# Kernel optimization log

Measured on AMD Instinct MI355X. Metric: run time of the kernel, lower is better.

Reference implementation:

```python
import jax, jax.numpy as jnp
import numpy as np

N = 50000          # nodes
E = 1600000        # edges (avg degree 32)
D_IN = 128
D_OUT = 128
NEG_SLOPE = 0.01   # F.leaky_relu default (module ignores its negative_slope attr)


def setup_inputs() -> dict:
    key = jax.random.key(0)
    k = jax.random.split(key, 7)
    h = jax.random.normal(k[0], (N, D_IN), dtype=jnp.float32)
    embedding = jax.random.normal(k[1], (N, D_OUT), dtype=jnp.float32)
    # params (xavier-ish scaling)
    W_lin = jax.random.normal(k[2], (D_OUT, D_IN), dtype=jnp.float32) * (2.0 / (D_IN + D_OUT)) ** 0.5
    w_fc = jax.random.normal(k[3], (1, 2 * D_OUT), dtype=jnp.float32) * (2.0 / (2 * D_OUT + 1)) ** 0.5
    w_emb = jax.random.normal(k[4], (1, 2 * D_OUT), dtype=jnp.float32) * (2.0 / (2 * D_OUT + 1)) ** 0.5
    src = jax.random.randint(k[5], (E,), 0, N, dtype=jnp.int64 if jax.config.jax_enable_x64 else jnp.int32)
    dst = jax.random.randint(k[6], (E,), 0, N, dtype=jnp.int64 if jax.config.jax_enable_x64 else jnp.int32)
    return {"h": h, "embedding": embedding, "W_lin": W_lin, "w_fc": w_fc,
            "w_emb": w_emb, "src": src, "dst": dst}


def reference(h, embedding, W_lin, w_fc, w_emb, src, dst):
    n = h.shape[0]
    d = W_lin.shape[0]
    # z = lin(h): [N, out]
    z = h @ W_lin.T
    # attn_fc(cat(z_src, z_dst)) + attn_embed(cat(e_src, e_dst)) split into per-node
    # scalar scores so we gather [E] scalars instead of materializing [E, 2*out].
    s_fc_src = z @ w_fc[0, :d]            # [N]
    s_fc_dst = z @ w_fc[0, d:]            # [N]
    s_em_src = embedding @ w_emb[0, :d]   # [N]
    s_em_dst = embedding @ w_emb[0, d:]   # [N]
    a = (s_fc_src + s_em_src)[src] + (s_fc_dst + s_em_dst)[dst]   # [E]
    e = jnp.where(a > 0, a, NEG_SLOPE * a)  # leaky_relu, slope 0.01
    # segment softmax over incoming edges of each dst node
    m = jax.ops.segment_max(e, dst, num_segments=n)               # [N]
    e_exp = jnp.exp(e - m[dst])                                   # [E]
    denom = jax.ops.segment_sum(e_exp, dst, num_segments=n)       # [N]
    alpha = e_exp / denom[dst]                                    # [E]
    # weighted neighbor aggregation: h_out[v] = sum_{(u->v)} alpha * z[u]
    h_out = jax.ops.segment_sum(alpha[:, None] * z[src], dst, num_segments=n)
    return h_out
```

## Files before the change

kernel.cpp:

```cpp
#include <hip/hip_runtime.h>
#include <hip/hip_bf16.h>

#define D 128
#define BSH 7
#define BDST 128
#define NCH 256
#define CAP 6144

typedef __attribute__((ext_vector_type(8))) short short8;
typedef __attribute__((ext_vector_type(4))) float f32x4;

__device__ __forceinline__ unsigned short f2bf(float f) {
  unsigned u = __float_as_uint(f);
  unsigned r = (u + 0x7FFFu + ((u >> 16) & 1u)) >> 16;
  return (unsigned short)r;
}

__global__ __launch_bounds__(256) void k_wconv(const float* __restrict__ W,
                                               unsigned short* __restrict__ Wb) {
  const int i = blockIdx.x * 256 + threadIdx.x;
  float4 f = ((const float4*)W)[i];
  ushort4 o;
  o.x = f2bf(f.x); o.y = f2bf(f.y); o.z = f2bf(f.z); o.w = f2bf(f.w);
  ((ushort4*)Wb)[i] = o;
}

__global__ __launch_bounds__(256) void k_lin(const float* __restrict__ h,
                                             const unsigned short* __restrict__ Wb,
                                             const float* __restrict__ w_fc,
                                             unsigned* __restrict__ zd,
                                             float* __restrict__ sfc_s,
                                             float* __restrict__ sfc_d, int n) {
  const int lane = threadIdx.x & 63;
  const int wid = threadIdx.x >> 6;
  const int m0 = blockIdx.x * 64 + wid * 16;
  if (m0 >= n) return;
  const int c = lane & 15;
  const int g = lane >> 4;

  int arow = m0 + c;
  if (arow >= n) arow = n - 1;
  const float4* hrow = (const float4*)(h + (size_t)arow * 128);

  short8 afr[4];
#pragma unroll
  for (int s = 0; s < 4; ++s) {
    float4 f0 = hrow[8 * s + 2 * g];
    float4 f1 = hrow[8 * s + 2 * g + 1];
    short8 a;
    a[0] = (short)f2bf(f0.x); a[1] = (short)f2bf(f0.y);
    a[2] = (short)f2bf(f0.z); a[3] = (short)f2bf(f0.w);
    a[4] = (short)f2bf(f1.x); a[5] = (short)f2bf(f1.y);
    a[6] = (short)f2bf(f1.z); a[7] = (short)f2bf(f1.w);
    afr[s] = a;
  }

  f32x4 acc[8];
#pragma unroll
  for (int t = 0; t < 8; ++t) acc[t] = (f32x4){0.f, 0.f, 0.f, 0.f};

#pragma unroll
  for (int s = 0; s < 4; ++s) {
#pragma unroll
    for (int t = 0; t < 8; ++t) {
      short8 b = *(const short8*)(Wb + ((size_t)(t * 16 + c) * 128 + 32 * s + 8 * g));
      acc[t] = __builtin_amdgcn_mfma_f32_16x16x32_bf16(afr[s], b, acc[t], 0, 0, 0);
    }
  }

  float wfs[8], wfd[8];
#pragma unroll
  for (int t = 0; t < 8; ++t) {
    wfs[t] = w_fc[t * 16 + c];
    wfd[t] = w_fc[128 + t * 16 + c];
  }

  const int rbase = m0 + 4 * g;
#pragma unroll
  for (int r = 0; r < 4; ++r) {
    const int row = rbase + r;
    if (row < n) {
#pragma unroll
      for (int tp = 0; tp < 4; ++tp) {
        unsigned dw = ((unsigned)f2bf(acc[tp + 4][r]) << 16) | (unsigned)f2bf(acc[tp][r]);
        zd[(size_t)row * 64 + tp * 16 + c] = dw;
      }
    }
    float ps = 0.f, pd = 0.f;
#pragma unroll
    for (int t = 0; t < 8; ++t) {
      ps += acc[t][r] * wfs[t];
      pd += acc[t][r] * wfd[t];
    }
#pragma unroll
    for (int off = 1; off < 16; off <<= 1) {
      ps += __shfl_xor(ps, off, 64);
      pd += __shfl_xor(pd, off, 64);
    }
    if (c == 0 && row < n) {
      sfc_s[row] = ps;
      sfc_d[row] = pd;
    }
  }
}

__global__ __launch_bounds__(256) void k_scal(const float* __restrict__ emb,
                                              const float* __restrict__ w_emb,
                                              const float* __restrict__ sfc_s,
                                              const float* __restrict__ sfc_d,
                                              float* __restrict__ a_src,
                                              float* __restrict__ a_dst, int n) {
  const int lane = threadIdx.x & 63;
  const int v = blockIdx.x * 4 + (threadIdx.x >> 6);
  if (v >= n) return;
  float2 ee = ((const float2*)emb)[(size_t)v * 64 + lane];
  float2 wes = ((const float2*)w_emb)[lane];
  float2 wed = ((const float2*)w_emb)[64 + lane];
  float ssrc = ee.x * wes.x + ee.y * wes.y;
  float sdst = ee.x * wed.x + ee.y * wed.y;
#pragma unroll
  for (int off = 32; off; off >>= 1) {
    ssrc += __shfl_xor(ssrc, off, 64);
    sdst += __shfl_xor(sdst, off, 64);
  }
  if (lane == 0) {
    a_src[v] = ssrc + sfc_s[v];
    a_dst[v] = sdst + sfc_d[v];
  }
}

__global__ __launch_bounds__(256) void k_chist(const int* __restrict__ dst,
                                               int* __restrict__ cnt,
                                               int E, int NB, int CHSZ) {
  __shared__ int hl[512];
  const int tid = threadIdx.x, c = blockIdx.x;
  for (int i = tid; i < NB; i += 256) hl[i] = 0;
  __syncthreads();
  const int beg = c * CHSZ, end = min(beg + CHSZ, E);
  for (int i = beg + tid; i < end; i += 256) atomicAdd(&hl[dst[i] >> BSH], 1);
  __syncthreads();
  for (int b = tid; b < NB; b += 256) cnt[(size_t)b * NCH + c] = hl[b];
}

__global__ __launch_bounds__(256) void ks1(const int* __restrict__ cnt,
                                           int* __restrict__ partial, int M) {
  const int tid = threadIdx.x;
  const int t0 = blockIdx.x * 1024 + tid * 4;
  int s = 0;
  if (t0 + 3 < M) {
    int4 v = *(const int4*)(cnt + t0);
    s = v.x + v.y + v.z + v.w;
  } else {
    for (int j = 0; j < 4; ++j)
      if (t0 + j < M) s += cnt[t0 + j];
  }
#pragma unroll
  for (int off = 32; off; off >>= 1) s += __shfl_xor(s, off, 64);
  __shared__ int w[4];
  if ((tid & 63) == 0) w[tid >> 6] = s;
  __syncthreads();
  if (tid == 0) partial[blockIdx.x] = w[0] + w[1] + w[2] + w[3];
}

__global__ __launch_bounds__(256) void ks2(const int* __restrict__ partial,
                                           int* __restrict__ chunk_off, int P) {
  __shared__ int s[256];
  const int tid = threadIdx.x;
  int v = (tid < P) ? partial[tid] : 0;
  s[tid] = v;
  __syncthreads();
  for (int off = 1; off < 256; off <<= 1) {
    int a = (tid >= off) ? s[tid - off] : 0;
    __syncthreads();
    s[tid] += a;
    __syncthreads();
  }
  if (tid < P) chunk_off[tid] = s[tid] - v;
}

__global__ __launch_bounds__(256) void ks3(int* __restrict__ cnt,
                                           const int* __restrict__ chunk_off, int M) {
  const int tid = threadIdx.x;
  const int t0 = blockIdx.x * 1024 + tid * 4;
  int v[4];
  int s = 0;
#pragma unroll
  for (int j = 0; j < 4; ++j) {
    v[j] = (t0 + j < M) ? cnt[t0 + j] : 0;
    s += v[j];
  }
  __shared__ int sh[256];
  sh[tid] = s;
  __syncthreads();
  for (int off = 1; off < 256; off <<= 1) {
    int a = (tid >= off) ? sh[tid - off] : 0;
    __syncthreads();
    sh[tid] += a;
    __syncthreads();
  }
  int excl = chunk_off[blockIdx.x] + sh[tid] - s;
#pragma unroll
  for (int j = 0; j < 4; ++j) {
    if (t0 + j < M) cnt[t0 + j] = excl;
    excl += v[j];
  }
}

__global__ __launch_bounds__(256) void k_cscat(const int* __restrict__ src,
                                               const int* __restrict__ dst,
                                               const int* __restrict__ S,
                                               unsigned* __restrict__ binrec,
                                               int E, int NB, int CHSZ) {
  __shared__ int cur[512];
  const int tid = threadIdx.x, c = blockIdx.x;
  for (int b = tid; b < NB; b += 256) cur[b] = S[(size_t)b * NCH + c];
  __syncthreads();
  const int beg = c * CHSZ, end = min(beg + CHSZ, E);
  for (int i = beg + tid; i < end; i += 256) {
    int d = dst[i];
    int pos = atomicAdd(&cur[d >> BSH], 1);
    binrec[pos] = ((unsigned)src[i] << BSH) | (unsigned)(d & (BDST - 1));
  }
}

__global__ __launch_bounds__(256) void k_build(const unsigned* __restrict__ binrec,
                                               const int* __restrict__ S,
                                               int* __restrict__ row,
                                               int* __restrict__ csr,
                                               int n, int E, int NB) {
  __shared__ unsigned rec[CAP];
  __shared__ int hist[BDST], cur[BDST], sc[BDST];
  const int tid = threadIdx.x, b = blockIdx.x;
  const int base = S[(size_t)b * NCH];
  const int next = (b + 1 < NB) ? S[(size_t)(b + 1) * NCH] : E;
  const int cntb = next - base;
  if (tid < BDST) hist[tid] = 0;
  __syncthreads();
  for (int i = tid; i < cntb; i += 256) {
    unsigned r = binrec[base + i];
    if (i < CAP) rec[i] = r;
    atomicAdd(&hist[r & (BDST - 1)], 1);
  }
  __syncthreads();
  if (tid < BDST) sc[tid] = hist[tid];
  __syncthreads();
  for (int off = 1; off < BDST; off <<= 1) {
    int a = (tid < BDST && tid >= off) ? sc[tid - off] : 0;
    __syncthreads();
    if (tid < BDST) sc[tid] += a;
    __syncthreads();
  }
  if (tid < BDST) {
    int excl = sc[tid] - hist[tid];
    cur[tid] = excl;
    int v = b * BDST + tid;
    if (v < n) row[v] = base + excl;
  }
  if (b == NB - 1 && tid == 0) row[n] = E;
  __syncthreads();
  for (int i = tid; i < cntb; i += 256) {
    unsigned r = (i < CAP) ? rec[i] : binrec[base + i];
    int dl = r & (BDST - 1);
    int pos = base + atomicAdd(&cur[dl], 1);
    csr[pos] = (int)(r >> BSH);
  }
}

__global__ __launch_bounds__(256) void k_agg(const unsigned* __restrict__ zd,
                                             const float* __restrict__ a_src,
                                             const float* __restrict__ a_dst,
                                             const int* __restrict__ row,
                                             const int* __restrict__ csr,
                                             float* __restrict__ out, int n) {
  const int lane = threadIdx.x & 63;
  const int grp = lane >> 4;
  const int sub = lane & 15;
  const int v = blockIdx.x * 4 + (threadIdx.x >> 6);
  if (v >= n) return;
  const int beg = row[v], end = row[v + 1];
  const float adv = a_dst[v];

  float accf[8];
#pragma unroll
  for (int j = 0; j < 8; ++j) accf[j] = 0.f;
  float ews = 0.f;

#pragma unroll 2
  for (int i = beg + grp; i < end; i += 4) {
    const int u = csr[i];
    const float a = a_src[u] + adv;
    const float e = a > 0.f ? a : 0.01f * a;
    const float ew = __expf(e);
    const uint4 zz = ((const uint4*)zd)[(size_t)u * 16 + sub];
    ews += ew;
    accf[0] += ew * __uint_as_float(zz.x << 16);
    accf[1] += ew * __uint_as_float(zz.x & 0xffff0000u);
    accf[2] += ew * __uint_as_float(zz.y << 16);
    accf[3] += ew * __uint_as_float(zz.y & 0xffff0000u);
    accf[4] += ew * __uint_as_float(zz.z << 16);
    accf[5] += ew * __uint_as_float(zz.z & 0xffff0000u);
    accf[6] += ew * __uint_as_float(zz.w << 16);
    accf[7] += ew * __uint_as_float(zz.w & 0xffff0000u);
  }

#pragma unroll
  for (int off = 16; off <= 32; off <<= 1) {
    ews += __shfl_xor(ews, off, 64);
#pragma unroll
    for (int j = 0; j < 8; ++j) accf[j] += __shfl_xor(accf[j], off, 64);
  }

  if (grp == 0) {
    const float inv = (end > beg) ? 1.f / ews : 0.f;
    float4 olo = make_float4(accf[0] * inv, accf[2] * inv, accf[4] * inv, accf[6] * inv);
    float4 ohi = make_float4(accf[1] * inv, accf[3] * inv, accf[5] * inv, accf[7] * inv);
    ((float4*)out)[(size_t)v * 32 + sub] = olo;
    ((float4*)out)[(size_t)v * 32 + 16 + sub] = ohi;
  }
}

extern "C" void kernel_launch(void* const* d_in, const int* in_sizes, int n_in,
                              void* d_out, int out_size, void* d_ws, size_t ws_size,
                              hipStream_t stream) {
  const float* h = (const float*)d_in[0];
  const float* emb = (const float*)d_in[1];
  const float* W = (const float*)d_in[2];
  const float* wfc = (const float*)d_in[3];
  const float* wemb = (const float*)d_in[4];
  const int* src = (const int*)d_in[5];
  const int* dst = (const int*)d_in[6];
  const int n = in_sizes[0] / D;
  const int E = in_sizes[5];
  const int NB = (n + BDST - 1) >> BSH;
  const int CHSZ = (E + NCH - 1) / NCH;
  const int M = NB * NCH;
  const int G1 = (M + 1023) / 1024;

  char* ws = (char*)d_ws;
  size_t off = 0;
  auto alloc = [&](size_t bytes) {
    void* p = ws + off;
    off = (off + bytes + 255) & ~(size_t)255;
    return p;
  };
  unsigned* zd = (unsigned*)alloc((size_t)n * 64 * 4);
  unsigned short* Wb = (unsigned short*)alloc(D * D * 2);
  float* sfc_s = (float*)alloc((size_t)n * 4);
  float* sfc_d = (float*)alloc((size_t)n * 4);
  float* a_src = (float*)alloc((size_t)n * 4);
  float* a_dst = (float*)alloc((size_t)n * 4);
  int* cnt = (int*)alloc((size_t)M * 4);
  int* partial = (int*)alloc((size_t)G1 * 4);
  int* chunk_off = (int*)alloc((size_t)G1 * 4);
  int* row = (int*)alloc((size_t)(n + 1) * 4);
  unsigned* binrec = (unsigned*)alloc((size_t)E * 4);
  int* csr = (int*)alloc((size_t)E * 4);
  (void)off;
  (void)ws_size;

  k_wconv<<<(D * D / 4 + 255) / 256, 256, 0, stream>>>(W, Wb);
  k_lin<<<(n + 63) / 64, 256, 0, stream>>>(h, Wb, wfc, zd, sfc_s, sfc_d, n);
  k_scal<<<(n + 3) / 4, 256, 0, stream>>>(emb, wemb, sfc_s, sfc_d, a_src, a_dst, n);
  k_chist<<<NCH, 256, 0, stream>>>(dst, cnt, E, NB, CHSZ);
  ks1<<<G1, 256, 0, stream>>>(cnt, partial, M);
  ks2<<<1, 256, 0, stream>>>(partial, chunk_off, G1);
  ks3<<<G1, 256, 0, stream>>>(cnt, chunk_off, M);
  k_cscat<<<NCH, 256, 0, stream>>>(src, dst, cnt, binrec, E, NB, CHSZ);
  k_build<<<NB, 256, 0, stream>>>(binrec, cnt, row, csr, n, E, NB);
  k_agg<<<(n + 3) / 4, 256, 0, stream>>>(zd, a_src, a_dst, row, csr, (float*)d_out, n);
}
```

Baseline: 141.9 us.

## Fuse embedding scores into linear kernel and CSR build into aggregation

After: 173.0 us. +21.9%, slower.

```diff
diff --git a/kernel.cpp b/kernel.cpp
--- a/kernel.cpp
+++ b/kernel.cpp
@@ -28,9 +28,12 @@
 __global__ __launch_bounds__(256) void k_lin(const float* __restrict__ h,
                                              const unsigned short* __restrict__ Wb,
                                              const float* __restrict__ w_fc,
+                                             const float* __restrict__ emb,
+                                             const float* __restrict__ w_emb,
                                              unsigned* __restrict__ zd,
-                                             float* __restrict__ sfc_s,
-                                             float* __restrict__ sfc_d, int n) {
+                                             float* __restrict__ a_src,
+                                             float* __restrict__ a_dst, int n) {
+  __shared__ float sfs[4][16], sfd[4][16];
   const int lane = threadIdx.x & 63;
   const int wid = threadIdx.x >> 6;
   const int m0 = blockIdx.x * 64 + wid * 16;
@@ -97,35 +100,33 @@
       ps += __shfl_xor(ps, off, 64);
       pd += __shfl_xor(pd, off, 64);
     }
-    if (c == 0 && row < n) {
-      sfc_s[row] = ps;
-      sfc_d[row] = pd;
-    }
-  }
-}
-
-__global__ __launch_bounds__(256) void k_scal(const float* __restrict__ emb,
-                                              const float* __restrict__ w_emb,
-                                              const float* __restrict__ sfc_s,
-                                              const float* __restrict__ sfc_d,
-                                              float* __restrict__ a_src,
-                                              float* __restrict__ a_dst, int n) {
-  const int lane = threadIdx.x & 63;
-  const int v = blockIdx.x * 4 + (threadIdx.x >> 6);
-  if (v >= n) return;
-  float2 ee = ((const float2*)emb)[(size_t)v * 64 + lane];
-  float2 wes = ((const float2*)w_emb)[lane];
-  float2 wed = ((const float2*)w_emb)[64 + lane];
-  float ssrc = ee.x * wes.x + ee.y * wes.y;
-  float sdst = ee.x * wed.x + ee.y * wed.y;
-#pragma unroll
-  for (int off = 32; off; off >>= 1) {
-    ssrc += __shfl_xor(ssrc, off, 64);
-    sdst += __shfl_xor(sdst, off, 64);
-  }
-  if (lane == 0) {
-    a_src[v] = ssrc + sfc_s[v];
-    a_dst[v] = sdst + sfc_d[v];
+    if (c == 0) {
+      sfs[wid][4 * g + r] = ps;
+      sfd[wid][4 * g + r] = pd;
+    }
+  }
+  __syncthreads();
+
+  const int nloc = lane >> 2;
+  const int qc = lane & 3;
+  const int node2 = m0 + nloc;
+  float es = 0.f, ed = 0.f;
+  if (node2 < n) {
+    const float4* er = (const float4*)(emb + (size_t)node2 * 128 + qc * 32);
+    const float4* wsp = (const float4*)(w_emb + qc * 32);
+    const float4* wdp = (const float4*)(w_emb + 128 + qc * 32);
+#pragma unroll
+    for (int j = 0; j < 8; ++j) {
+      float4 e4 = er[j], s4 = wsp[j], d4 = wdp[j];
+      es += e4.x * s4.x + e4.y * s4.y + e4.z * s4.z + e4.w * s4.w;
+      ed += e4.x * d4.x + e4.y * d4.y + e4.z * d4.z + e4.w * d4.w;
+    }
+  }
+  es += __shfl_xor(es, 1, 64); es += __shfl_xor(es, 2, 64);
+  ed += __shfl_xor(ed, 1, 64); ed += __shfl_xor(ed, 2, 64);
+  if (qc == 0 && node2 < n) {
+    a_src[node2] = es + sfs[wid][nloc];
+    a_dst[node2] = ed + sfd[wid][nloc];
   }
 }
 
@@ -223,99 +224,94 @@
   }
 }
 
-__global__ __launch_bounds__(256) void k_build(const unsigned* __restrict__ binrec,
-                                               const int* __restrict__ S,
-                                               int* __restrict__ row,
-                                               int* __restrict__ csr,
-                                               int n, int E, int NB) {
-  __shared__ unsigned rec[CAP];
-  __shared__ int hist[BDST], cur[BDST], sc[BDST];
+__global__ __launch_bounds__(256) void k_bagg(const unsigned* __restrict__ binrec,
+                                              const int* __restrict__ S,
+                                              const unsigned* __restrict__ zd,
+                                              const float* __restrict__ a_src,
+                                              const float* __restrict__ a_dst,
+                                              float* __restrict__ out,
+                                              int n, int E, int NB) {
+  __shared__ int csrl[CAP];
+  __shared__ int hist[BDST];
+  __shared__ int lrow[BDST];
+  __shared__ int cur[BDST];
   const int tid = threadIdx.x, b = blockIdx.x;
   const int base = S[(size_t)b * NCH];
   const int next = (b + 1 < NB) ? S[(size_t)(b + 1) * NCH] : E;
   const int cntb = next - base;
+
   if (tid < BDST) hist[tid] = 0;
+  __syncthreads();
+  for (int i = tid; i < cntb; i += 256)
+    atomicAdd(&hist[binrec[base + i] & (BDST - 1)], 1);
+  __syncthreads();
+  if (tid < BDST) lrow[tid] = hist[tid];
+  __syncthreads();
+  for (int off = 1; off < BDST; off <<= 1) {
+    int a = (tid < BDST && tid >= off) ? lrow[tid - off] : 0;
+    __syncthreads();
+    if (tid < BDST) lrow[tid] += a;
+    __syncthreads();
+  }
+  if (tid < BDST) cur[tid] = lrow[tid] - hist[tid];
   __syncthreads();
   for (int i = tid; i < cntb; i += 256) {
     unsigned r = binrec[base + i];
-    if (i < CAP) rec[i] = r;
-    atomicAdd(&hist[r & (BDST - 1)], 1);
-  }
-  __syncthreads();
-  if (tid < BDST) sc[tid] = hist[tid];
-  __syncthreads();
-  for (int off = 1; off < BDST; off <<= 1) {
-    int a = (tid < BDST && tid >= off) ? sc[tid - off] : 0;
-    __syncthreads();
-    if (tid < BDST) sc[tid] += a;
-    __syncthreads();
-  }
-  if (tid < BDST) {
-    int excl = sc[tid] - hist[tid];
-    cur[tid] = excl;
-    int v = b * BDST + tid;
-    if (v < n) row[v] = base + excl;
-  }
-  if (b == NB - 1 && tid == 0) row[n] = E;
-  __syncthreads();
-  for (int i = tid; i < cntb; i += 256) {
-    unsigned r = (i < CAP) ? rec[i] : binrec[base + i];
-    int dl = r & (BDST - 1);
-    int pos = base + atomicAdd(&cur[dl], 1);
-    csr[pos] = (int)(r >> BSH);
-  }
-}
-
-__global__ __launch_bounds__(256) void k_agg(const unsigned* __restrict__ zd,
-                                             const float* __restrict__ a_src,
-                                             const float* __restrict__ a_dst,
-                                             const int* __restrict__ row,
-                                             const int* __restrict__ csr,
-                                             float* __restrict__ out, int n) {
-  const int lane = threadIdx.x & 63;
+    int pos = atomicAdd(&cur[r & (BDST - 1)], 1);
+    csrl[pos] = (int)(r >> BSH);
+  }
+  __syncthreads();
+
+  const int lane = tid & 63;
+  const int wid = tid >> 6;
   const int grp = lane >> 4;
   const int sub = lane & 15;
-  const int v = blockIdx.x * 4 + (threadIdx.x >> 6);
-  if (v >= n) return;
-  const int beg = row[v], end = row[v + 1];
-  const float adv = a_dst[v];
-
-  float accf[8];
-#pragma unroll
-  for (int j = 0; j < 8; ++j) accf[j] = 0.f;
-  float ews = 0.f;
+
+  for (int k = 0; k < 32; ++k) {
+    const int dl = wid * 32 + k;
+    const int v = b * BDST + dl;
+    if (v >= n) break;
+    const int end = lrow[dl];
+    const int beg = end - hist[dl];
+    const float adv = a_dst[v];
+
+    float accf[8];
+#pragma unroll
+    for (int j = 0; j < 8; ++j) accf[j] = 0.f;
+    float ews = 0.f;
 
 #pragma unroll 2
-  for (int i = beg + grp; i < end; i += 4) {
-    const int u = csr[i];
-    const float a = a_src[u] + adv;
-    const float e = a > 0.f ? a : 0.01f * a;
-    const float ew = __expf(e);
-    const uint4 zz = ((const uint4*)zd)[(size_t)u * 16 + sub];
-    ews += ew;
-    accf[0] += ew * __uint_as_float(zz.x << 16);
-    accf[1] += ew * __uint_as_float(zz.x & 0xffff0000u);
-    accf[2] += ew * __uint_as_float(zz.y << 16);
-    accf[3] += ew * __uint_as_float(zz.y & 0xffff0000u);
-    accf[4] += ew * __uint_as_float(zz.z << 16);
-    accf[5] += ew * __uint_as_float(zz.z & 0xffff0000u);
-    accf[6] += ew * __uint_as_float(zz.w << 16);
-    accf[7] += ew * __uint_as_float(zz.w & 0xffff0000u);
-  }
-
-#pragma unroll
-  for (int off = 16; off <= 32; off <<= 1) {
-    ews += __shfl_xor(ews, off, 64);
-#pragma unroll
-    for (int j = 0; j < 8; ++j) accf[j] += __shfl_xor(accf[j], off, 64);
-  }
-
-  if (grp == 0) {
-    const float inv = (end > beg) ? 1.f / ews : 0.f;
-    float4 olo = make_float4(accf[0] * inv, accf[2] * inv, accf[4] * inv, accf[6] * inv);
-    float4 ohi = make_float4(accf[1] * inv, accf[3] * inv, accf[5] * inv, accf[7] * inv);
-    ((float4*)out)[(size_t)v * 32 + sub] = olo;
-    ((float4*)out)[(size_t)v * 32 + 16 + sub] = ohi;
+    for (int i = beg + grp; i < end; i += 4) {
+      const int u = csrl[i];
+      const float a = a_src[u] + adv;
+      const float e = a > 0.f ? a : 0.01f * a;
+      const float ew = __expf(e);
+      const uint4 zz = ((const uint4*)zd)[(size_t)u * 16 + sub];
+      ews += ew;
+      accf[0] += ew * __uint_as_float(zz.x << 16);
+      accf[1] += ew * __uint_as_float(zz.x & 0xffff0000u);
+      accf[2] += ew * __uint_as_float(zz.y << 16);
+      accf[3] += ew * __uint_as_float(zz.y & 0xffff0000u);
+      accf[4] += ew * __uint_as_float(zz.z << 16);
+      accf[5] += ew * __uint_as_float(zz.z & 0xffff0000u);
+      accf[6] += ew * __uint_as_float(zz.w << 16);
+      accf[7] += ew * __uint_as_float(zz.w & 0xffff0000u);
+    }
+
+#pragma unroll
+    for (int off = 16; off <= 32; off <<= 1) {
+      ews += __shfl_xor(ews, off, 64);
+#pragma unroll
+      for (int j = 0; j < 8; ++j) accf[j] += __shfl_xor(accf[j], off, 64);
+    }
+
+    if (grp == 0) {
+      const float inv = (end > beg) ? 1.f / ews : 0.f;
+      float4 olo = make_float4(accf[0] * inv, accf[2] * inv, accf[4] * inv, accf[6] * inv);
+      float4 ohi = make_float4(accf[1] * inv, accf[3] * inv, accf[5] * inv, accf[7] * inv);
+      ((float4*)out)[(size_t)v * 32 + sub] = olo;
+      ((float4*)out)[(size_t)v * 32 + 16 + sub] = ohi;
+    }
   }
 }
 
@@ -345,27 +341,21 @@
   };
   unsigned* zd = (unsigned*)alloc((size_t)n * 64 * 4);
   unsigned short* Wb = (unsigned short*)alloc(D * D * 2);
-  float* sfc_s = (float*)alloc((size_t)n * 4);
-  float* sfc_d = (float*)alloc((size_t)n * 4);
   float* a_src = (float*)alloc((size_t)n * 4);
   float* a_dst = (float*)alloc((size_t)n * 4);
   int* cnt = (int*)alloc((size_t)M * 4);
   int* partial = (int*)alloc((size_t)G1 * 4);
   int* chunk_off = (int*)alloc((size_t)G1 * 4);
-  int* row = (int*)alloc((size_t)(n + 1) * 4);
   unsigned* binrec = (unsigned*)alloc((size_t)E * 4);
-  int* csr = (int*)alloc((size_t)E * 4);
   (void)off;
   (void)ws_size;
 
   k_wconv<<<(D * D / 4 + 255) / 256, 256, 0, stream>>>(W, Wb);
-  k_lin<<<(n + 63) / 64, 256, 0, stream>>>(h, Wb, wfc, zd, sfc_s, sfc_d, n);
-  k_scal<<<(n + 3) / 4, 256, 0, stream>>>(emb, wemb, sfc_s, sfc_d, a_src, a_dst, n);
+  k_lin<<<(n + 63) / 64, 256, 0, stream>>>(h, Wb, wfc, emb, wemb, zd, a_src, a_dst, n);
   k_chist<<<NCH, 256, 0, stream>>>(dst, cnt, E, NB, CHSZ);
   ks1<<<G1, 256, 0, stream>>>(cnt, partial, M);
   ks2<<<1, 256, 0, stream>>>(partial, chunk_off, G1);
   ks3<<<G1, 256, 0, stream>>>(cnt, chunk_off, M);
   k_cscat<<<NCH, 256, 0, stream>>>(src, dst, cnt, binrec, E, NB, CHSZ);
-  k_build<<<NB, 256, 0, stream>>>(binrec, cnt, row, csr, n, E, NB);
-  k_agg<<<(n + 3) / 4, 256, 0, stream>>>(zd, a_src, a_dst, row, csr, (float*)d_out, n);
-}
+  k_bagg<<<NB, 256, 0, stream>>>(binrec, cnt, zd, a_src, a_dst, (float*)d_out, n, E, NB);
+}
```
